# Optimization experiments

Hardware: AMD Instinct MI355X
Metric: run time of the kernel (lower is better)

Reference implementation:

```python
import jax, jax.numpy as jnp
import numpy as np

N = 50000
E = 800000
IN = 256
H = 4
C = 64
HC = H * C
LAT = 64
EPS = 1e-5
NEG_SLOPE = 0.2


def setup_inputs() -> dict:
    key = jax.random.key(0)
    ks = jax.random.split(key, 20)
    g = lambda k, shape, fan: jax.random.normal(k, shape, jnp.float32) * (1.0 / np.sqrt(fan))
    return {
        "x": jax.random.normal(ks[0], (N, IN), jnp.float32),
        "edge_index": jax.random.randint(ks[1], (2, E), 0, N, jnp.int32),
        "Wl1": g(ks[2], (IN, HC), IN), "Wr1": g(ks[3], (IN, HC), IN),
        "att1": g(ks[4], (H, C), C), "b1": jnp.zeros((HC,), jnp.float32),
        "ln1_g": jnp.ones((HC,), jnp.float32), "ln1_b": jnp.zeros((HC,), jnp.float32),
        "Wl2": g(ks[5], (HC, HC), HC), "Wr2": g(ks[6], (HC, HC), HC),
        "att2": g(ks[7], (H, C), C), "b2": jnp.zeros((HC,), jnp.float32),
        "ln2_g": jnp.ones((HC,), jnp.float32), "ln2_b": jnp.zeros((HC,), jnp.float32),
        "Wmu": g(ks[8], (HC, LAT), HC), "bmu": jnp.zeros((LAT,), jnp.float32),
        "Wlv": g(ks[9], (HC, LAT), HC), "blv": jnp.zeros((LAT,), jnp.float32),
    }


def _gatv2_layer(x, src, dst, Wl, Wr, att, bias):
    # GATv2: e_ij = att . leaky_relu(Wl x_j + Wr x_i); segment softmax over dst; aggregate Wl x_j
    xl = (x @ Wl).reshape(-1, H, C)  # source transform [N,H,C]
    xr = (x @ Wr).reshape(-1, H, C)  # target transform [N,H,C]
    e = jax.nn.leaky_relu(xl[src] + xr[dst], NEG_SLOPE)   # [E',H,C]
    score = jnp.einsum('ehc,hc->eh', e, att)              # [E',H]
    m = jax.ops.segment_max(score, dst, num_segments=N)   # [N,H]
    ex = jnp.exp(score - m[dst])
    denom = jax.ops.segment_sum(ex, dst, num_segments=N)  # [N,H]
    alpha = ex / denom[dst]                               # self-loops guarantee denom > 0
    out = jax.ops.segment_sum(alpha[:, :, None] * xl[src], dst, num_segments=N)  # [N,H,C]
    return out.reshape(-1, HC) + bias


def _layernorm(x, g, b):
    mu = jnp.mean(x, axis=-1, keepdims=True)
    var = jnp.mean((x - mu) ** 2, axis=-1, keepdims=True)
    return (x - mu) * jax.lax.rsqrt(var + EPS) * g + b


def reference(x, edge_index, Wl1, Wr1, att1, b1, ln1_g, ln1_b,
              Wl2, Wr2, att2, b2, ln2_g, ln2_b, Wmu, bmu, Wlv, blv):
    loops = jnp.arange(N, dtype=edge_index.dtype)
    src = jnp.concatenate([edge_index[0], loops])  # add_self_loops=True
    dst = jnp.concatenate([edge_index[1], loops])
    h = _gatv2_layer(x, src, dst, Wl1, Wr1, att1, b1)
    h = jax.nn.elu(_layernorm(h, ln1_g, ln1_b))  # dropout is identity in eval mode
    h = _gatv2_layer(h, src, dst, Wl2, Wr2, att2, b2)
    h = jax.nn.elu(_layernorm(h, ln2_g, ln2_b))
    mu = h @ Wmu + bmu
    logvar = h @ Wlv + blv
    return mu, logvar
```

## Files before the change

### kernel.cpp

```cpp
#include <hip/hip_runtime.h>
#include <hip/hip_bf16.h>

#define NN 50000
#define NE 800000
#define HCn 256
#define LATn 64

typedef short bf16x4 __attribute__((ext_vector_type(4)));
typedef short bf16x8 __attribute__((ext_vector_type(8)));
typedef float f32x4 __attribute__((ext_vector_type(4)));

__device__ __forceinline__ short f2b(float f) {
    __hip_bfloat16 h = __float2bfloat16(f);
    return __builtin_bit_cast(short, h);
}
__device__ __forceinline__ float b2f(short s) {
    return __bfloat162float(__builtin_bit_cast(__hip_bfloat16, s));
}

#define SWZF(v, pat) __builtin_bit_cast(float, __builtin_amdgcn_ds_swizzle(__builtin_bit_cast(int, v), pat))

__global__ void hist_kernel(const int* __restrict__ dst, int* __restrict__ counts) {
    int e = blockIdx.x * 256 + threadIdx.x;
    if (e < NE) atomicAdd(&counts[dst[e]], 1);
}

__global__ __launch_bounds__(1024) void scan1_kernel(int* __restrict__ counts,
                                                     int* __restrict__ blocksum) {
    const int g = blockIdx.x * 1024 + threadIdx.x;
    const int lane = threadIdx.x & 63;
    const int wv = threadIdx.x >> 6;
    int v = (g < NN) ? counts[g] : 0;
    int s = v;
#pragma unroll
    for (int d = 1; d < 64; d <<= 1) {
        int t = __shfl_up(s, d, 64);
        if (lane >= d) s += t;
    }
    __shared__ int wsum[16];
    if (lane == 63) wsum[wv] = s;
    __syncthreads();
    if (threadIdx.x == 0) {
        int run = 0;
#pragma unroll
        for (int q = 0; q < 16; ++q) { int t = wsum[q]; wsum[q] = run; run += t; }
        blocksum[blockIdx.x] = run;
    }
    __syncthreads();
    int excl = s - v + wsum[wv];
    if (g < NN) counts[g] = excl;
}

__global__ void scan2_kernel(int* __restrict__ blocksum, int* __restrict__ offsets, int nblk) {
    const int lane = threadIdx.x;
    int v = (lane < nblk) ? blocksum[lane] : 0;
    int s = v;
#pragma unroll
    for (int d = 1; d < 64; d <<= 1) {
        int t = __shfl_up(s, d, 64);
        if (lane >= d) s += t;
    }
    if (lane < nblk) blocksum[lane] = s - v;
    if (lane == 0) offsets[NN] = NE;
}

__global__ __launch_bounds__(1024) void scan3_kernel(const int* __restrict__ counts,
                                                     const int* __restrict__ blocksum,
                                                     int* __restrict__ offsets,
                                                     int* __restrict__ cursor) {
    const int g = blockIdx.x * 1024 + threadIdx.x;
    if (g < NN) {
        int v = counts[g] + blocksum[blockIdx.x];
        offsets[g] = v;
        cursor[g]  = v;
    }
}

__global__ void scatter_kernel(const int* __restrict__ src, const int* __restrict__ dst,
                               int* __restrict__ cursor, int* __restrict__ csr_src) {
    int e = blockIdx.x * 256 + threadIdx.x;
    if (e < NE) {
        int p = atomicAdd(&cursor[dst[e]], 1);
        csr_src[p] = src[e];
    }
}

__global__ __launch_bounds__(256) void cvt_x_kernel(const float* __restrict__ x,
                                                    short* __restrict__ xb) {
    long i = ((long)blockIdx.x * 256 + threadIdx.x) * 8;
    const f32x4* p = reinterpret_cast<const f32x4*>(x + i);
    f32x4 a = p[0], b = p[1];
    bf16x8 o;
#pragma unroll
    for (int j = 0; j < 4; ++j) { o[j] = f2b(a[j]); o[4 + j] = f2b(b[j]); }
    *reinterpret_cast<bf16x8*>(xb + i) = o;
}

__global__ void pack_w_kernel(const float* __restrict__ Wl1, const float* __restrict__ Wr1,
                              const float* __restrict__ Wl2, const float* __restrict__ Wr2,
                              const float* __restrict__ Wmu, const float* __restrict__ Wlv,
                              const float* __restrict__ bmu, const float* __restrict__ blv,
                              short* __restrict__ Wb1t, short* __restrict__ Wb2t,
                              short* __restrict__ Wb3t, float* __restrict__ bias3) {
    int i = blockIdx.x * 256 + threadIdx.x;
    const int S1 = 512 * 256, S2 = 2 * S1, S3 = S2 + 128 * 256;
    if (i < S1) {
        int c = i >> 8, k = i & 255;
        float v = (c < 256) ? Wl1[k * 256 + c] : Wr1[k * 256 + (c - 256)];
        Wb1t[i] = f2b(v);
    } else if (i < S2) {
        int j = i - S1; int c = j >> 8, k = j & 255;
        float v = (c < 256) ? Wl2[k * 256 + c] : Wr2[k * 256 + (c - 256)];
        Wb2t[j] = f2b(v);
    } else if (i < S3) {
        int j = i - S2; int c = j >> 8, k = j & 255;
        float v = (c < 64) ? Wmu[k * 64 + c] : Wlv[k * 64 + (c - 64)];
        Wb3t[j] = f2b(v);
    } else if (i < S3 + 128) {
        int c = i - S3;
        bias3[c] = (c < 64) ? bmu[c] : blv[c - 64];
    }
}

template<int OUT_MODE>
__global__ __launch_bounds__(256) void gemm_k(
    const short* __restrict__ A, const short* __restrict__ Wbt,
    void* __restrict__ outp, const float* __restrict__ bias, int Nc)
{
    __shared__ short Bs[64 * 264];
    const int t = threadIdx.x;
    const int w = t >> 6, lane = t & 63;
    const int row0 = blockIdx.x * 128, col0 = blockIdx.y * 64;

    {
        const int sn = t >> 2;
        const int sk0 = (t & 3) * 8;
        const short* wp = Wbt + (long)(col0 + sn) * 256 + sk0;
#pragma unroll
        for (int r = 0; r < 8; ++r) {
            int k = r * 32 + sk0;
            bf16x8 v = *reinterpret_cast<const bf16x8*>(wp + r * 32);
            *reinterpret_cast<bf16x8*>(&Bs[sn * 264 + k]) = v;
        }
    }
    __syncthreads();

    f32x4 acc[2][4];
#pragma unroll
    for (int a = 0; a < 2; ++a)
#pragma unroll
        for (int b = 0; b < 4; ++b) acc[a][b] = (f32x4){0.f, 0.f, 0.f, 0.f};

    const int arow = lane & 15, kq = lane >> 4;
    int r0 = row0 + w * 32 + arow;      if (r0 > NN - 1) r0 = NN - 1;
    int r1 = row0 + w * 32 + 16 + arow; if (r1 > NN - 1) r1 = NN - 1;
    const short* pa0 = A + (long)r0 * 256 + kq * 8;
    const short* pa1 = A + (long)r1 * 256 + kq * 8;

#pragma unroll
    for (int k0 = 0; k0 < 256; k0 += 32) {
        bf16x8 a0 = *reinterpret_cast<const bf16x8*>(pa0 + k0);
        bf16x8 a1 = *reinterpret_cast<const bf16x8*>(pa1 + k0);
#pragma unroll
        for (int nt = 0; nt < 4; ++nt) {
            bf16x8 b = *reinterpret_cast<const bf16x8*>(&Bs[(nt * 16 + arow) * 264 + k0 + kq * 8]);
            acc[0][nt] = __builtin_amdgcn_mfma_f32_16x16x32_bf16(a0, b, acc[0][nt], 0, 0, 0);
            acc[1][nt] = __builtin_amdgcn_mfma_f32_16x16x32_bf16(a1, b, acc[1][nt], 0, 0, 0);
        }
    }

#pragma unroll
    for (int rb = 0; rb < 2; ++rb)
#pragma unroll
        for (int nt = 0; nt < 4; ++nt) {
            int gcol = col0 + nt * 16 + arow;
#pragma unroll
            for (int r = 0; r < 4; ++r) {
                int grow = row0 + w * 32 + rb * 16 + kq * 4 + r;
                if (grow < NN) {
                    float v = acc[rb][nt][r];
                    if (OUT_MODE == 0) {
                        ((short*)outp)[(long)grow * Nc + gcol] = f2b(v);
                    } else {
                        v += bias[gcol];
                        float* o = (float*)outp;
                        if (gcol < 64) o[(long)grow * 64 + gcol] = v;
                        else           o[(long)NN * 64 + (long)grow * 64 + (gcol - 64)] = v;
                    }
                }
            }
        }
}

__device__ __forceinline__ void edge_score(const short* __restrict__ xlr, int j, int c4,
                                           const float* xr, const f32x4& attv,
                                           float* xf, float& s) {
    bf16x4 v = *reinterpret_cast<const bf16x4*>(xlr + (long)j * 512 + c4);
    s = 0.f;
#pragma unroll
    for (int k = 0; k < 4; ++k) {
        xf[k] = b2f(v[k]);
        float val = xf[k] + xr[k];
        val = fmaxf(val, 0.2f * val);
        s = fmaf(val, attv[k], s);
    }
    s += SWZF(s, 0x041F);
    s += SWZF(s, 0x081F);
    s += SWZF(s, 0x101F);
    s += SWZF(s, 0x201F);
}

__global__ __launch_bounds__(256) void gat_node_kernel(
    const short* __restrict__ xlr,
    const int* __restrict__ offsets, const int* __restrict__ csr_src,
    const float* __restrict__ att, const float* __restrict__ bias,
    const float* __restrict__ ln_g, const float* __restrict__ ln_b,
    short* __restrict__ hout)
{
    const int i = blockIdx.x * 4 + (threadIdx.x >> 6);
    const int lane = threadIdx.x & 63;
    const int c4 = (lane >> 4) * 64 + (lane & 15) * 4;

    f32x4 attv = *reinterpret_cast<const f32x4*>(att + c4);
    float xr[4];
    {
        bf16x4 v = *reinterpret_cast<const bf16x4*>(xlr + (long)i * 512 + 256 + c4);
#pragma unroll
        for (int k = 0; k < 4; ++k) xr[k] = b2f(v[k]);
    }

    float m, l;
    float acc[4];
    {
        float xf[4], s;
        edge_score(xlr, i, c4, xr, attv, xf, s);
        m = s; l = 1.f;
#pragma unroll
        for (int k = 0; k < 4; ++k) acc[k] = xf[k];
    }

    const int p0 = offsets[i], p1 = offsets[i + 1];
    int p = p0;
    for (; p + 2 <= p1; p += 2) {
        int ja = __builtin_amdgcn_readfirstlane(csr_src[p]);
        int jb = __builtin_amdgcn_readfirstlane(csr_src[p + 1]);
        float xa[4], xb[4], sa, sb;
        edge_score(xlr, ja, c4, xr, attv, xa, sa);
        edge_score(xlr, jb, c4, xr, attv, xb, sb);
        float sm = fmaxf(sa, sb);
        if (__all(sm <= m + 4.f)) {
            float exa = __expf(sa - m), exb = __expf(sb - m);
            l += exa + exb;
#pragma unroll
            for (int k = 0; k < 4; ++k)
                acc[k] += exa * xa[k] + exb * xb[k];
        } else {
            float mn = fmaxf(m, sm);
            float corr = __expf(m - mn);
            float exa = __expf(sa - mn), exb = __expf(sb - mn);
            l = fmaf(l, corr, exa + exb);
#pragma unroll
            for (int k = 0; k < 4; ++k)
                acc[k] = fmaf(acc[k], corr, exa * xa[k] + exb * xb[k]);
            m = mn;
        }
    }
    if (p < p1) {
        int ja = __builtin_amdgcn_readfirstlane(csr_src[p]);
        float xa[4], sa;
        edge_score(xlr, ja, c4, xr, attv, xa, sa);
        if (__all(sa <= m + 4.f)) {
            float exa = __expf(sa - m);
            l += exa;
#pragma unroll
            for (int k = 0; k < 4; ++k) acc[k] += exa * xa[k];
        } else {
            float mn = fmaxf(m, sa);
            float corr = __expf(m - mn);
            float exa = __expf(sa - mn);
            l = fmaf(l, corr, exa);
#pragma unroll
            for (int k = 0; k < 4; ++k) acc[k] = fmaf(acc[k], corr, exa * xa[k]);
            m = mn;
        }
    }

    float inv = 1.f / l;
    f32x4 bv = *reinterpret_cast<const f32x4*>(bias + c4);
    float out[4], s1 = 0.f, s2 = 0.f;
#pragma unroll
    for (int k = 0; k < 4; ++k) {
        out[k] = acc[k] * inv + bv[k];
        s1 += out[k];
        s2 += out[k] * out[k];
    }
    s1 += SWZF(s1, 0x041F); s2 += SWZF(s2, 0x041F);
    s1 += SWZF(s1, 0x081F); s2 += SWZF(s2, 0x081F);
    s1 += SWZF(s1, 0x101F); s2 += SWZF(s2, 0x101F);
    s1 += SWZF(s1, 0x201F); s2 += SWZF(s2, 0x201F);
    s1 += SWZF(s1, 0x401F); s2 += SWZF(s2, 0x401F);
    s1 += __shfl_xor(s1, 32, 64);
    s2 += __shfl_xor(s2, 32, 64);
    float mu  = s1 * (1.f / 256.f);
    float var = s2 * (1.f / 256.f) - mu * mu;
    float rs  = rsqrtf(var + 1e-5f);
    f32x4 gv  = *reinterpret_cast<const f32x4*>(ln_g + c4);
    f32x4 bbv = *reinterpret_cast<const f32x4*>(ln_b + c4);
    bf16x4 o;
#pragma unroll
    for (int k = 0; k < 4; ++k) {
        float y = (out[k] - mu) * rs * gv[k] + bbv[k];
        y = y > 0.f ? y : expm1f(y);
        o[k] = f2b(y);
    }
    *reinterpret_cast<bf16x4*>(hout + (long)i * 256 + c4) = o;
}

extern "C" void kernel_launch(void* const* d_in, const int* in_sizes, int n_in,
                              void* d_out, int out_size, void* d_ws, size_t ws_size,
                              hipStream_t stream) {
    const float* x    = (const float*)d_in[0];
    const int*   ei   = (const int*)d_in[1];
    const float* Wl1  = (const float*)d_in[2];
    const float* Wr1  = (const float*)d_in[3];
    const float* att1 = (const float*)d_in[4];
    const float* b1   = (const float*)d_in[5];
    const float* ln1g = (const float*)d_in[6];
    const float* ln1b = (const float*)d_in[7];
    const float* Wl2  = (const float*)d_in[8];
    const float* Wr2  = (const float*)d_in[9];
    const float* att2 = (const float*)d_in[10];
    const float* b2   = (const float*)d_in[11];
    const float* ln2g = (const float*)d_in[12];
    const float* ln2b = (const float*)d_in[13];
    const float* Wmu  = (const float*)d_in[14];
    const float* bmu  = (const float*)d_in[15];
    const float* Wlv  = (const float*)d_in[16];
    const float* blv  = (const float*)d_in[17];

    short* bufXL = (short*)d_ws;
    short* bufH  = bufXL + (long)NN * 512;
    short* Wb1t  = bufH + (long)NN * 256;
    short* Wb2t  = Wb1t + 512 * 256;
    short* Wb3t  = Wb2t + 512 * 256;
    float* bias3 = (float*)(Wb3t + 128 * 256);
    int* counts  = (int*)(bias3 + 128);
    int* offsets = counts + NN;
    int* cursor  = offsets + NN + 1;
    int* csr_src = cursor + NN;
    int* blocksum = csr_src + NE;

    const int* src = ei;
    const int* dst = ei + NE;

    const int NBLK = (NN + 1023) / 1024;

    hipMemsetAsync(counts, 0, NN * sizeof(int), stream);
    hist_kernel<<<(NE + 255) / 256, 256, 0, stream>>>(dst, counts);
    scan1_kernel<<<NBLK, 1024, 0, stream>>>(counts, blocksum);
    scan2_kernel<<<1, 64, 0, stream>>>(blocksum, offsets, NBLK);
    scan3_kernel<<<NBLK, 1024, 0, stream>>>(counts, blocksum, offsets, cursor);
    scatter_kernel<<<(NE + 255) / 256, 256, 0, stream>>>(src, dst, cursor, csr_src);

    cvt_x_kernel<<<(NN * HCn) / (8 * 256), 256, 0, stream>>>(x, bufH);
    pack_w_kernel<<<1153, 256, 0, stream>>>(Wl1, Wr1, Wl2, Wr2, Wmu, Wlv, bmu, blv,
                                            Wb1t, Wb2t, Wb3t, bias3);

    const int GM = (NN + 127) / 128;
    dim3 g1(GM, 8);
    dim3 g3(GM, 2);

    gemm_k<0><<<g1, 256, 0, stream>>>(bufH, Wb1t, bufXL, nullptr, 512);
    gat_node_kernel<<<NN / 4, 256, 0, stream>>>(bufXL, offsets, csr_src,
                                                att1, b1, ln1g, ln1b, bufH);
    gemm_k<0><<<g1, 256, 0, stream>>>(bufH, Wb2t, bufXL, nullptr, 512);
    gat_node_kernel<<<NN / 4, 256, 0, stream>>>(bufXL, offsets, csr_src,
                                                att2, b2, ln2g, ln2b, bufH);
    gemm_k<1><<<g3, 256, 0, stream>>>(bufH, Wb3t, d_out, bias3, 128);
}
```

Measured before the change: 386.3 us.

## Decompose leaky-relu score into abs term plus per-node precomputed linear terms

```diff
diff --git a/kernel.cpp b/kernel.cpp
--- a/kernel.cpp
+++ b/kernel.cpp
@@ -19,6 +19,10 @@
 }
 
 #define SWZF(v, pat) __builtin_bit_cast(float, __builtin_amdgcn_ds_swizzle(__builtin_bit_cast(int, v), pat))
+
+#define C04L2E 0.5770780163555854f
+#define C06L2E 0.8656170245333781f
+#define DEFER_THR 8.0f
 
 __global__ void hist_kernel(const int* __restrict__ dst, int* __restrict__ counts) {
     int e = blockIdx.x * 256 + threadIdx.x;
@@ -192,26 +196,43 @@
         }
 }
 
-__device__ __forceinline__ void edge_score(const short* __restrict__ xlr, int j, int c4,
-                                           const float* xr, const f32x4& attv,
-                                           float* xf, float& s) {
-    bf16x4 v = *reinterpret_cast<const bf16x4*>(xlr + (long)j * 512 + c4);
-    s = 0.f;
-#pragma unroll
-    for (int k = 0; k < 4; ++k) {
-        xf[k] = b2f(v[k]);
-        float val = xf[k] + xr[k];
-        val = fmaxf(val, 0.2f * val);
-        s = fmaf(val, attv[k], s);
-    }
+__global__ __launch_bounds__(256) void att_pre_kernel(
+    const short* __restrict__ xlr, const float* __restrict__ att, float* __restrict__ a)
+{
+    const int i = blockIdx.x * 4 + (threadIdx.x >> 6);
+    const int lane = threadIdx.x & 63;
+    const int c4 = (lane >> 4) * 64 + (lane & 15) * 4;
+    f32x4 attv = *reinterpret_cast<const f32x4*>(att + c4);
+    bf16x4 v = *reinterpret_cast<const bf16x4*>(xlr + (long)i * 512 + c4);
+    float s = 0.f;
+#pragma unroll
+    for (int k = 0; k < 4; ++k) s = fmaf(b2f(v[k]), attv[k], s);
     s += SWZF(s, 0x041F);
     s += SWZF(s, 0x081F);
     s += SWZF(s, 0x101F);
     s += SWZF(s, 0x201F);
+    if ((lane & 15) == 0) a[i * 4 + (lane >> 4)] = s * C06L2E;
+}
+
+__device__ __forceinline__ void edge_abs_score(const short* __restrict__ xlr, int j, int c4,
+                                               const float* xr, const f32x4& attv04,
+                                               float* xf, float& s) {
+    bf16x4 v = *reinterpret_cast<const bf16x4*>(xlr + (long)j * 512 + c4);
+    s = 0.f;
+#pragma unroll
+    for (int k = 0; k < 4; ++k) {
+        xf[k] = b2f(v[k]);
+        float vv = xf[k] + xr[k];
+        s = fmaf(attv04[k], fabsf(vv), s);
+    }
+    s += SWZF(s, 0x041F);
+    s += SWZF(s, 0x081F);
+    s += SWZF(s, 0x101F);
+    s += SWZF(s, 0x201F);
 }
 
 __global__ __launch_bounds__(256) void gat_node_kernel(
-    const short* __restrict__ xlr,
+    const short* __restrict__ xlr, const float* __restrict__ aarr,
     const int* __restrict__ offsets, const int* __restrict__ csr_src,
     const float* __restrict__ att, const float* __restrict__ bias,
     const float* __restrict__ ln_g, const float* __restrict__ ln_b,
@@ -219,9 +240,13 @@
 {
     const int i = blockIdx.x * 4 + (threadIdx.x >> 6);
     const int lane = threadIdx.x & 63;
-    const int c4 = (lane >> 4) * 64 + (lane & 15) * 4;
-
-    f32x4 attv = *reinterpret_cast<const f32x4*>(att + c4);
+    const int h  = lane >> 4;
+    const int c4 = h * 64 + (lane & 15) * 4;
+
+    f32x4 attv04 = *reinterpret_cast<const f32x4*>(att + c4);
+#pragma unroll
+    for (int k = 0; k < 4; ++k) attv04[k] *= C04L2E;
+
     float xr[4];
     {
         bf16x4 v = *reinterpret_cast<const bf16x4*>(xlr + (long)i * 512 + 256 + c4);
@@ -232,55 +257,73 @@
     float m, l;
     float acc[4];
     {
+        float aj = aarr[i * 4 + h];
         float xf[4], s;
-        edge_score(xlr, i, c4, xr, attv, xf, s);
-        m = s; l = 1.f;
+        edge_abs_score(xlr, i, c4, xr, attv04, xf, s);
+        m = s + aj; l = 1.f;
 #pragma unroll
         for (int k = 0; k < 4; ++k) acc[k] = xf[k];
     }
 
     const int p0 = offsets[i], p1 = offsets[i + 1];
     int p = p0;
-    for (; p + 2 <= p1; p += 2) {
-        int ja = __builtin_amdgcn_readfirstlane(csr_src[p]);
-        int jb = __builtin_amdgcn_readfirstlane(csr_src[p + 1]);
-        float xa[4], xb[4], sa, sb;
-        edge_score(xlr, ja, c4, xr, attv, xa, sa);
-        edge_score(xlr, jb, c4, xr, attv, xb, sb);
-        float sm = fmaxf(sa, sb);
-        if (__all(sm <= m + 4.f)) {
-            float exa = __expf(sa - m), exb = __expf(sb - m);
-            l += exa + exb;
+    for (; p + 4 <= p1; p += 4) {
+        int jl = csr_src[p + (lane & 3)];
+        int j0 = __builtin_amdgcn_readlane(jl, 0);
+        int j1 = __builtin_amdgcn_readlane(jl, 1);
+        int j2 = __builtin_amdgcn_readlane(jl, 2);
+        int j3 = __builtin_amdgcn_readlane(jl, 3);
+        float a0 = aarr[j0 * 4 + h], a1 = aarr[j1 * 4 + h];
+        float a2 = aarr[j2 * 4 + h], a3 = aarr[j3 * 4 + h];
+        float x0[4], x1[4], x2[4], x3[4], s0, s1, s2, s3;
+        edge_abs_score(xlr, j0, c4, xr, attv04, x0, s0);
+        edge_abs_score(xlr, j1, c4, xr, attv04, x1, s1);
+        edge_abs_score(xlr, j2, c4, xr, attv04, x2, s2);
+        edge_abs_score(xlr, j3, c4, xr, attv04, x3, s3);
+        s0 += a0; s1 += a1; s2 += a2; s3 += a3;
+        float sm = fmaxf(fmaxf(s0, s1), fmaxf(s2, s3));
+        if (__all(sm <= m + DEFER_THR)) {
+            float e0 = __builtin_amdgcn_exp2f(s0 - m);
+            float e1 = __builtin_amdgcn_exp2f(s1 - m);
+            float e2 = __builtin_amdgcn_exp2f(s2 - m);
+            float e3 = __builtin_amdgcn_exp2f(s3 - m);
+            l += (e0 + e1) + (e2 + e3);
 #pragma unroll
             for (int k = 0; k < 4; ++k)
-                acc[k] += exa * xa[k] + exb * xb[k];
+                acc[k] = fmaf(e0, x0[k], fmaf(e1, x1[k], fmaf(e2, x2[k], fmaf(e3, x3[k], acc[k]))));
         } else {
             float mn = fmaxf(m, sm);
-            float corr = __expf(m - mn);
-            float exa = __expf(sa - mn), exb = __expf(sb - mn);
-            l = fmaf(l, corr, exa + exb);
+            float corr = __builtin_amdgcn_exp2f(m - mn);
+            float e0 = __builtin_amdgcn_exp2f(s0 - mn);
+            float e1 = __builtin_amdgcn_exp2f(s1 - mn);
+            float e2 = __builtin_amdgcn_exp2f(s2 - mn);
+            float e3 = __builtin_amdgcn_exp2f(s3 - mn);
+            l = fmaf(l, corr, (e0 + e1) + (e2 + e3));
 #pragma unroll
             for (int k = 0; k < 4; ++k)
-                acc[k] = fmaf(acc[k], corr, exa * xa[k] + exb * xb[k]);
+                acc[k] = fmaf(acc[k], corr,
+                         fmaf(e0, x0[k], fmaf(e1, x1[k], fmaf(e2, x2[k], e3 * x3[k]))));
             m = mn;
         }
     }
-    if (p < p1) {
-        int ja = __builtin_amdgcn_readfirstlane(csr_src[p]);
+    for (; p < p1; ++p) {
+        int j = __builtin_amdgcn_readfirstlane(csr_src[p]);
+        float aj = aarr[j * 4 + h];
         float xa[4], sa;
-        edge_score(xlr, ja, c4, xr, attv, xa, sa);
-        if (__all(sa <= m + 4.f)) {
-            float exa = __expf(sa - m);
-            l += exa;
-#pragma unroll
-            for (int k = 0; k < 4; ++k) acc[k] += exa * xa[k];
+        edge_abs_score(xlr, j, c4, xr, attv04, xa, sa);
+        sa += aj;
+        if (__all(sa <= m + DEFER_THR)) {
+            float ex = __builtin_amdgcn_exp2f(sa - m);
+            l += ex;
+#pragma unroll
+            for (int k = 0; k < 4; ++k) acc[k] = fmaf(ex, xa[k], acc[k]);
         } else {
             float mn = fmaxf(m, sa);
-            float corr = __expf(m - mn);
-            float exa = __expf(sa - mn);
-            l = fmaf(l, corr, exa);
-#pragma unroll
-            for (int k = 0; k < 4; ++k) acc[k] = fmaf(acc[k], corr, exa * xa[k]);
+            float corr = __builtin_amdgcn_exp2f(m - mn);
+            float ex = __builtin_amdgcn_exp2f(sa - mn);
+            l = fmaf(l, corr, ex);
+#pragma unroll
+            for (int k = 0; k < 4; ++k) acc[k] = fmaf(acc[k], corr, ex * xa[k]);
             m = mn;
         }
     }
@@ -349,6 +392,7 @@
     int* cursor  = offsets + NN + 1;
     int* csr_src = cursor + NN;
     int* blocksum = csr_src + NE;
+    float* a_arr = (float*)(blocksum + 64);
 
     const int* src = ei;
     const int* dst = ei + NE;
@@ -371,10 +415,12 @@
     dim3 g3(GM, 2);
 
     gemm_k<0><<<g1, 256, 0, stream>>>(bufH, Wb1t, bufXL, nullptr, 512);
-    gat_node_kernel<<<NN / 4, 256, 0, stream>>>(bufXL, offsets, csr_src,
+    att_pre_kernel<<<NN / 4, 256, 0, stream>>>(bufXL, att1, a_arr);
+    gat_node_kernel<<<NN / 4, 256, 0, stream>>>(bufXL, a_arr, offsets, csr_src,
                                                 att1, b1, ln1g, ln1b, bufH);
     gemm_k<0><<<g1, 256, 0, stream>>>(bufH, Wb2t, bufXL, nullptr, 512);
-    gat_node_kernel<<<NN / 4, 256, 0, stream>>>(bufXL, offsets, csr_src,
+    att_pre_kernel<<<NN / 4, 256, 0, stream>>>(bufXL, att2, a_arr);
+    gat_node_kernel<<<NN / 4, 256, 0, stream>>>(bufXL, a_arr, offsets, csr_src,
                                                 att2, b2, ln2g, ln2b, bufH);
     gemm_k<1><<<g3, 256, 0, stream>>>(bufH, Wb3t, d_out, bias3, 128);
 }
```

Measured after the change: 380.6 us. About the same (-1.5%).
